# Optimization experiments

Hardware: AMD Instinct MI355X
Metric: run time of the kernel (lower is better)

Reference implementation:

```python
import jax, jax.numpy as jnp
import numpy as np

N_NODES = 100000
N_EDGES = 1600000
IN_C, HID_C, OUT_C = 64, 64, 40


def setup_inputs() -> dict:
    key = jax.random.key(0)
    ks = jax.random.split(key, 8)
    x = jax.random.normal(ks[0], (N_NODES, IN_C), dtype=jnp.float32)
    edge_index = jax.random.randint(ks[1], (2, N_EDGES), 0, N_NODES, dtype=jnp.int32)
    s = 1.0 / np.sqrt(HID_C)
    W1 = jax.random.uniform(ks[2], (IN_C, HID_C), jnp.float32, -s, s)
    b1 = jnp.zeros((HID_C,), jnp.float32)
    Wh = jax.random.uniform(ks[3], (HID_C, HID_C), jnp.float32, -s, s)
    bh = jnp.zeros((HID_C,), jnp.float32)
    W2 = jax.random.uniform(ks[4], (HID_C, OUT_C), jnp.float32, -s, s)
    b2 = jnp.zeros((OUT_C,), jnp.float32)
    return {"x": x, "edge_index": edge_index, "W1": W1, "b1": b1,
            "Wh": Wh, "bh": bh, "W2": W2, "b2": b2}


def reference(x, edge_index, W1, b1, Wh, bh, W2, b2):
    N = x.shape[0]
    loop = jnp.arange(N, dtype=edge_index.dtype)
    # GCN normalization with self-loops: A_hat = D^-1/2 (A + I) D^-1/2
    src = jnp.concatenate([edge_index[0], loop])  # [E + N]
    dst = jnp.concatenate([edge_index[1], loop])
    deg = jax.ops.segment_sum(jnp.ones_like(dst, dtype=x.dtype), dst, num_segments=N)
    dinv = jnp.where(deg > 0, jax.lax.rsqrt(deg), 0.0)
    norm = dinv[src] * dinv[dst]  # [E + N]

    def gcn_conv(h, W, b):
        h = h @ W                              # [N, out]
        msg = h[src] * norm[:, None]           # gather + scale, [E+N, out]
        return jax.ops.segment_sum(msg, dst, num_segments=N) + b

    h = jax.nn.relu(gcn_conv(x, W1, b1))       # conv1 (dropout = identity in eval)
    h = jax.nn.relu(gcn_conv(h, Wh, bh))       # hidden_conv, layer_size=2 -> one pass
    h = gcn_conv(h, W2, b2)                    # conv2
    return jax.nn.log_softmax(h, axis=1)
```

## Files before the change

kernel.cpp:

```cpp
#include <hip/hip_runtime.h>
#include <hip/hip_bf16.h>
#include <math.h>

#define EPT 16
#define BCAP 16384

typedef _Float16 half8 __attribute__((ext_vector_type(8)));
typedef _Float16 half2v __attribute__((ext_vector_type(2)));
typedef float f32x4 __attribute__((ext_vector_type(4)));

__device__ __forceinline__ unsigned short f16r(float f) {
    _Float16 h = (_Float16)f;
    return __builtin_bit_cast(unsigned short, h);
}
__device__ __forceinline__ half2v h2(unsigned u) {
    return __builtin_bit_cast(half2v, u);
}


__global__ void scat1_kernel(const int* __restrict__ src, const int* __restrict__ dst,
                             int* __restrict__ cntg, unsigned* __restrict__ ebuf, int E) {
    __shared__ int lh[256];
    __shared__ int lbase[256];
    int tid = threadIdx.x;
    lh[tid] = 0;
    __syncthreads();
    int base = blockIdx.x * (256 * EPT);
    int ds[EPT], ss[EPT];
#pragma unroll
    for (int k = 0; k < EPT; ++k) {
        int e = base + k * 256 + tid;
        ds[k] = (e < E) ? dst[e] : -1;
        ss[k] = (e < E) ? src[e] : 0;
    }
#pragma unroll
    for (int k = 0; k < EPT; ++k) {
        if (ds[k] >= 0) atomicAdd(&lh[ds[k] >> 9], 1);
    }
    __syncthreads();
    if (lh[tid] > 0) lbase[tid] = atomicAdd(&cntg[tid], lh[tid]);
    lh[tid] = 0;
    __syncthreads();
#pragma unroll
    for (int k = 0; k < EPT; ++k) {
        if (ds[k] >= 0) {
            int b = ds[k] >> 9;
            int pos = lbase[b] + atomicAdd(&lh[b], 1);
            ebuf[(size_t)b * BCAP + pos] = ((unsigned)ss[k] << 9) | (unsigned)(ds[k] & 511);
        }
    }
}

__global__ void build_kernel(const unsigned* __restrict__ ebuf, const int* __restrict__ cntg,
                             int* __restrict__ row_ptr, int* __restrict__ col,
                             float* __restrict__ dinv, int N, int E) {
    __shared__ int deg[512];
    __shared__ int sh[256];
    int b = blockIdx.x;
    int tid = threadIdx.x;

    int v = cntg[tid];
    sh[tid] = v;
    __syncthreads();
    int val = v;
    for (int off = 1; off < 256; off <<= 1) {
        int add = 0;
        if (tid >= off) add = sh[tid - off];
        __syncthreads();
        val += add;
        sh[tid] = val;
        __syncthreads();
    }
    int start = (b > 0) ? sh[b - 1] : 0;
    int cnt = cntg[b];
    __syncthreads();

    int nodeBase = b << 9;
    int nn = N - nodeBase;
    if (nn > 512) nn = 512;
    if (nn < 0) nn = 0;
    const unsigned* eb = ebuf + (size_t)b * BCAP;

    deg[tid] = 0;
    deg[tid + 256] = 0;
    __syncthreads();
    for (int j = tid; j < cnt; j += 256) {
        atomicAdd(&deg[eb[j] & 511u], 1);
    }
    __syncthreads();

    int i0 = tid * 2, i1 = i0 + 1;
    int v0 = deg[i0], v1 = deg[i1];
    int tot = v0 + v1;
    sh[tid] = tot;
    __syncthreads();
    int val2 = tot;
    for (int off = 1; off < 256; off <<= 1) {
        int add = 0;
        if (tid >= off) add = sh[tid - off];
        __syncthreads();
        val2 += add;
        sh[tid] = val2;
        __syncthreads();
    }
    int excl = val2 - tot;

    if (i0 < nn) { row_ptr[nodeBase + i0] = start + excl;      dinv[nodeBase + i0] = rsqrtf((float)v0 + 1.0f); }
    if (i1 < nn) { row_ptr[nodeBase + i1] = start + excl + v0; dinv[nodeBase + i1] = rsqrtf((float)v1 + 1.0f); }
    if (b == 0 && tid == 0) row_ptr[N] = E;
    deg[i0] = start + excl;
    deg[i1] = start + excl + v0;
    __syncthreads();

    for (int j = tid; j < cnt; j += 256) {
        unsigned rec = eb[j];
        int pos = atomicAdd(&deg[rec & 511u], 1);
        col[pos] = (int)(rec >> 9);
    }
}


__global__ void cvtpack_kernel(const float* __restrict__ x, unsigned short* __restrict__ xb,
                               int n4, int npad, const float* __restrict__ dinv,
                               const float* __restrict__ W1, const float* __restrict__ Wh,
                               const float* __restrict__ W2, unsigned short* __restrict__ wp1,
                               unsigned short* __restrict__ wph, unsigned short* __restrict__ wp2) {
    int bid = blockIdx.x;
    if (bid < 16) {
        int i = bid * 256 + threadIdx.x;
        int j = i & 7;
        int lane = (i >> 3) & 63;
        int hh = (i >> 9) & 1;
        int t = i >> 10;
        int k = hh * 32 + (lane >> 4) * 8 + j;
        int cc = t * 16 + (lane & 15);
        wp1[i] = f16r(W1[k * 64 + cc]);
        wph[i] = f16r(Wh[k * 64 + cc]);
        if (t < 3) wp2[i] = f16r(cc < 40 ? W2[k * 40 + cc] : 0.f);
    } else {
        if (bid == 16 && threadIdx.x < 8) {
            *(uint4*)(xb + (size_t)npad * 64 + threadIdx.x * 8) = make_uint4(0, 0, 0, 0);
        }
        int i = (bid - 16) * 256 + threadIdx.x;
        if (i < n4) {
            float dn = dinv[i >> 4];
            float4 v = *(const float4*)(x + (size_t)i * 4);
            ushort4 o;
            o.x = f16r(v.x * dn); o.y = f16r(v.y * dn);
            o.z = f16r(v.z * dn); o.w = f16r(v.w * dn);
            *(ushort4*)(xb + (size_t)i * 4) = o;
        }
    }
}


__launch_bounds__(256, 8)
__global__ void agg_kernel(const unsigned short* __restrict__ h, const int* __restrict__ row_ptr,
                           const int* __restrict__ col, const float* __restrict__ dinv,
                           unsigned short* __restrict__ aggout, int n, int zrow) {
    int tid = threadIdx.x;
    int lane = tid & 63;
    int node = blockIdx.x * 4 + (tid >> 6);
    if (node >= n) return;

    int sub = lane >> 3;
    unsigned choff = (lane & 7) * 16u;

    int beg = row_ptr[node];
    int deg = row_ptr[node + 1] - beg;
    float di = dinv[node];
    int total = deg + 1;

    half2v a0 = (half2v)0, a1 = (half2v)0, a2 = (half2v)0, a3 = (half2v)0;

    int base = 0;
    while (base < total) {
        int vi = base + lane;
        int idx = zrow;
        if (vi < deg) idx = col[beg + vi];
        else if (vi == deg) idx = node;
        int cnt = min(total - base, 64);
#pragma unroll
        for (int it = 0; it < 4; ++it) {
            int c0 = it * 16;
            if (c0 >= cnt) break;
            int s0 = __shfl(idx, c0 + sub);
            int s1 = __shfl(idx, c0 + 8 + sub);
            uint4 u0 = *(const uint4*)((const char*)h + (((unsigned)s0 << 7) + choff));
            uint4 u1 = *(const uint4*)((const char*)h + (((unsigned)s1 << 7) + choff));
            a0 += h2(u0.x);  a1 += h2(u0.y);  a2 += h2(u0.z);  a3 += h2(u0.w);
            a0 += h2(u1.x);  a1 += h2(u1.y);  a2 += h2(u1.z);  a3 += h2(u1.w);
        }
        base += cnt;
    }
#pragma unroll
    for (int off = 8; off <= 32; off <<= 1) {
        a0 += __builtin_bit_cast(half2v, __shfl_xor(__builtin_bit_cast(int, a0), off));
        a1 += __builtin_bit_cast(half2v, __shfl_xor(__builtin_bit_cast(int, a1), off));
        a2 += __builtin_bit_cast(half2v, __shfl_xor(__builtin_bit_cast(int, a2), off));
        a3 += __builtin_bit_cast(half2v, __shfl_xor(__builtin_bit_cast(int, a3), off));
    }

    if (sub == 0) {
        half2v dih = __builtin_bit_cast(half2v, __builtin_amdgcn_cvt_pkrtz(di, di));
        a0 *= dih; a1 *= dih; a2 *= dih; a3 *= dih;
        uint4 o;
        o.x = __builtin_bit_cast(unsigned, a0);
        o.y = __builtin_bit_cast(unsigned, a1);
        o.z = __builtin_bit_cast(unsigned, a2);
        o.w = __builtin_bit_cast(unsigned, a3);
        *(uint4*)((char*)aggout + (((unsigned)node << 7) + choff)) = o;
    }
}


__global__ void gemm_relu_kernel(const unsigned short* __restrict__ A,
                                 const unsigned short* __restrict__ wp,
                                 const float* __restrict__ bias,
                                 const float* __restrict__ dinv,
                                 unsigned short* __restrict__ out, int nTiles, int n, int zrow) {
    if (blockIdx.x == 0 && threadIdx.x < 8) {
        *(uint4*)(out + (size_t)zrow * 64 + threadIdx.x * 8) = make_uint4(0, 0, 0, 0);
    }
    int wv = blockIdx.x * 4 + (threadIdx.x >> 6);
    int lane = threadIdx.x & 63;
    if (wv >= nTiles) return;
    int q = lane >> 4, c = lane & 15;

    half8 bfrag[4][2];
#pragma unroll
    for (int t = 0; t < 4; ++t)
#pragma unroll
        for (int hh = 0; hh < 2; ++hh)
            bfrag[t][hh] = *(const half8*)(wp + t * 1024 + hh * 512 + lane * 8);
    float bs[4];
#pragma unroll
    for (int t = 0; t < 4; ++t) bs[t] = bias[t * 16 + c];

    int nodeBase = wv * 16;
    const unsigned short* arow = A + (size_t)(nodeBase + c) * 64 + q * 8;
    half8 a0 = *(const half8*)(arow);
    half8 a1 = *(const half8*)(arow + 32);

    f32x4 acc[4];
#pragma unroll
    for (int t = 0; t < 4; ++t) {
        f32x4 z = {0.f, 0.f, 0.f, 0.f};
        z = __builtin_amdgcn_mfma_f32_16x16x32_f16(a0, bfrag[t][0], z, 0, 0, 0);
        z = __builtin_amdgcn_mfma_f32_16x16x32_f16(a1, bfrag[t][1], z, 0, 0, 0);
        acc[t] = z;
    }

#pragma unroll
    for (int r = 0; r < 4; ++r) {
        int node = nodeBase + q * 4 + r;
        if (node < n) {
            float dn = dinv[node];
            unsigned short* orow = out + (size_t)node * 64;
#pragma unroll
            for (int t = 0; t < 4; ++t)
                orow[t * 16 + c] = f16r(fmaxf(acc[t][r] + bs[t], 0.f) * dn);
        }
    }
}

__global__ void gemm_lsm_kernel(const unsigned short* __restrict__ A,
                                const unsigned short* __restrict__ wp,
                                const float* __restrict__ bias,
                                float* __restrict__ out, int nTiles, int n) {
    int wv = blockIdx.x * 4 + (threadIdx.x >> 6);
    int lane = threadIdx.x & 63;
    if (wv >= nTiles) return;
    int q = lane >> 4, c = lane & 15;
    bool v2ok = (c < 8);

    half8 bfrag[3][2];
#pragma unroll
    for (int t = 0; t < 3; ++t)
#pragma unroll
        for (int hh = 0; hh < 2; ++hh)
            bfrag[t][hh] = *(const half8*)(wp + t * 1024 + hh * 512 + lane * 8);
    float bs[3];
    bs[0] = bias[c];
    bs[1] = bias[16 + c];
    bs[2] = v2ok ? bias[32 + c] : 0.f;

    int nodeBase = wv * 16;
    const unsigned short* arow = A + (size_t)(nodeBase + c) * 64 + q * 8;
    half8 a0 = *(const half8*)(arow);
    half8 a1 = *(const half8*)(arow + 32);

    f32x4 acc[3];
#pragma unroll
    for (int t = 0; t < 3; ++t) {
        f32x4 z = {0.f, 0.f, 0.f, 0.f};
        z = __builtin_amdgcn_mfma_f32_16x16x32_f16(a0, bfrag[t][0], z, 0, 0, 0);
        z = __builtin_amdgcn_mfma_f32_16x16x32_f16(a1, bfrag[t][1], z, 0, 0, 0);
        acc[t] = z;
    }

#pragma unroll
    for (int r = 0; r < 4; ++r) {
        int node = nodeBase + q * 4 + r;
        if (node < n) {
            float v0 = acc[0][r] + bs[0];
            float v1 = acc[1][r] + bs[1];
            float v2 = v2ok ? (acc[2][r] + bs[2]) : -INFINITY;
            float m = fmaxf(fmaxf(v0, v1), v2);
#pragma unroll
            for (int off = 1; off <= 8; off <<= 1) m = fmaxf(m, __shfl_xor(m, off));
            float s = expf(v0 - m) + expf(v1 - m) + (v2ok ? expf(v2 - m) : 0.f);
#pragma unroll
            for (int off = 1; off <= 8; off <<= 1) s += __shfl_xor(s, off);
            float ls = m + logf(s);
            float* orow = out + (size_t)node * 40;
            orow[c] = v0 - ls;
            orow[16 + c] = v1 - ls;
            if (v2ok) orow[32 + c] = v2 - ls;
        }
    }
}


extern "C" void kernel_launch(void* const* d_in, const int* in_sizes, int n_in,
                              void* d_out, int out_size, void* d_ws, size_t ws_size,
                              hipStream_t stream) {
    const float* x  = (const float*)d_in[0];
    const int* ei   = (const int*)d_in[1];
    const float* W1 = (const float*)d_in[2];
    const float* b1 = (const float*)d_in[3];
    const float* Wh = (const float*)d_in[4];
    const float* bh = (const float*)d_in[5];
    const float* W2 = (const float*)d_in[6];
    const float* b2 = (const float*)d_in[7];
    float* out = (float*)d_out;

    const int N = in_sizes[0] / 64;
    const int E = in_sizes[1] / 2;
    const int nbuk = (N + 511) >> 9;
    const int nTiles = (N + 15) / 16;
    const int Npad = nTiles * 16;

    const int* srcp = ei;
    const int* dstp = ei + E;

    size_t off = 0;
    auto alloc = [&](size_t bytes) {
        size_t o = off;
        off = (off + bytes + 255) & ~(size_t)255;
        return o;
    };
    char* ws = (char*)d_ws;
    int*      cntg    = (int*)(ws + alloc(256 * 4));
    int*      row_ptr = (int*)(ws + alloc((size_t)(N + 1) * 4));
    float*    dinv    = (float*)(ws + alloc((size_t)N * 4));
    int*      col     = (int*)(ws + alloc((size_t)E * 4));
    unsigned* ebuf    = (unsigned*)(ws + alloc((size_t)nbuk * BCAP * 4));
    unsigned short* wp1  = (unsigned short*)(ws + alloc(4096 * 2));
    unsigned short* wph  = (unsigned short*)(ws + alloc(4096 * 2));
    unsigned short* wp2  = (unsigned short*)(ws + alloc(3072 * 2));
    unsigned short* xb   = (unsigned short*)(ws + alloc((size_t)(Npad + 1) * 64 * 2));
    unsigned short* aggA = (unsigned short*)(ws + alloc((size_t)Npad * 64 * 2));
    unsigned short* gA   = (unsigned short*)(ws + alloc((size_t)(Npad + 1) * 64 * 2));
    (void)ws_size;

    hipMemsetAsync(cntg, 0, 256 * 4, stream);

    const int ebGrid = (E + 256 * EPT - 1) / (256 * EPT);
    scat1_kernel<<<ebGrid, 256, 0, stream>>>(srcp, dstp, cntg, ebuf, E);
    build_kernel<<<nbuk, 256, 0, stream>>>(ebuf, cntg, row_ptr, col, dinv, N, E);

    const int n4 = N * 16;
    cvtpack_kernel<<<16 + (n4 + 255) / 256, 256, 0, stream>>>(x, xb, n4, Npad, dinv,
                                                              W1, Wh, W2, wp1, wph, wp2);

    const int aggGrid = (N + 3) / 4;
    const int gemmGrid = (nTiles + 3) / 4;

    agg_kernel<<<aggGrid, 256, 0, stream>>>(xb, row_ptr, col, dinv, aggA, N, Npad);
    gemm_relu_kernel<<<gemmGrid, 256, 0, stream>>>(aggA, wp1, b1, dinv, gA, nTiles, N, Npad);
    agg_kernel<<<aggGrid, 256, 0, stream>>>(gA, row_ptr, col, dinv, aggA, N, Npad);
    gemm_relu_kernel<<<gemmGrid, 256, 0, stream>>>(aggA, wph, bh, dinv, gA, nTiles, N, Npad);
    agg_kernel<<<aggGrid, 256, 0, stream>>>(gA, row_ptr, col, dinv, aggA, N, Npad);
    gemm_lsm_kernel<<<gemmGrid, 256, 0, stream>>>(aggA, wp2, b2, out, nTiles, N);
}
```

Measured before the change: 269.8 us.

## Fuse neighbor aggregation with MFMA GEMM per 16-node tile via shared memory

Each block now aggregates 16 nodes (4 per wave, sequentially) into a shared-memory tile, then runs the MFMA projection with bias, ReLU or log-softmax directly from LDS. This removes the intermediate aggregated buffer round-trip through global memory and halves the number of kernel launches per layer. The trade-off is less memory-level parallelism per wave, since nodes are processed one after another, plus a block barrier. The final layer also leaves three of the four waves idle during the GEMM.

```diff
diff --git a/kernel.cpp b/kernel.cpp
--- a/kernel.cpp
+++ b/kernel.cpp
@@ -155,122 +155,169 @@
 
 
 __launch_bounds__(256, 8)
-__global__ void agg_kernel(const unsigned short* __restrict__ h, const int* __restrict__ row_ptr,
-                           const int* __restrict__ col, const float* __restrict__ dinv,
-                           unsigned short* __restrict__ aggout, int n, int zrow) {
+__global__ void fused_relu_kernel(const unsigned short* __restrict__ h,
+                                  const int* __restrict__ row_ptr,
+                                  const int* __restrict__ col,
+                                  const float* __restrict__ dinv,
+                                  const unsigned short* __restrict__ wp,
+                                  const float* __restrict__ bias,
+                                  unsigned short* __restrict__ out,
+                                  int n, int zrow) {
+    __shared__ unsigned short tile[16][72];
+    if (blockIdx.x == 0 && threadIdx.x < 8) {
+        *(uint4*)(out + (size_t)zrow * 64 + threadIdx.x * 8) = make_uint4(0, 0, 0, 0);
+    }
     int tid = threadIdx.x;
+    int w = tid >> 6;
     int lane = tid & 63;
-    int node = blockIdx.x * 4 + (tid >> 6);
-    if (node >= n) return;
-
     int sub = lane >> 3;
     unsigned choff = (lane & 7) * 16u;
-
-    int beg = row_ptr[node];
-    int deg = row_ptr[node + 1] - beg;
-    float di = dinv[node];
-    int total = deg + 1;
-
-    half2v a0 = (half2v)0, a1 = (half2v)0, a2 = (half2v)0, a3 = (half2v)0;
-
-    int base = 0;
-    while (base < total) {
-        int vi = base + lane;
-        int idx = zrow;
-        if (vi < deg) idx = col[beg + vi];
-        else if (vi == deg) idx = node;
-        int cnt = min(total - base, 64);
-#pragma unroll
-        for (int it = 0; it < 4; ++it) {
-            int c0 = it * 16;
-            if (c0 >= cnt) break;
-            int s0 = __shfl(idx, c0 + sub);
-            int s1 = __shfl(idx, c0 + 8 + sub);
-            uint4 u0 = *(const uint4*)((const char*)h + (((unsigned)s0 << 7) + choff));
-            uint4 u1 = *(const uint4*)((const char*)h + (((unsigned)s1 << 7) + choff));
-            a0 += h2(u0.x);  a1 += h2(u0.y);  a2 += h2(u0.z);  a3 += h2(u0.w);
-            a0 += h2(u1.x);  a1 += h2(u1.y);  a2 += h2(u1.z);  a3 += h2(u1.w);
-        }
-        base += cnt;
-    }
-#pragma unroll
-    for (int off = 8; off <= 32; off <<= 1) {
-        a0 += __builtin_bit_cast(half2v, __shfl_xor(__builtin_bit_cast(int, a0), off));
-        a1 += __builtin_bit_cast(half2v, __shfl_xor(__builtin_bit_cast(int, a1), off));
-        a2 += __builtin_bit_cast(half2v, __shfl_xor(__builtin_bit_cast(int, a2), off));
-        a3 += __builtin_bit_cast(half2v, __shfl_xor(__builtin_bit_cast(int, a3), off));
-    }
-
-    if (sub == 0) {
-        half2v dih = __builtin_bit_cast(half2v, __builtin_amdgcn_cvt_pkrtz(di, di));
-        a0 *= dih; a1 *= dih; a2 *= dih; a3 *= dih;
-        uint4 o;
-        o.x = __builtin_bit_cast(unsigned, a0);
-        o.y = __builtin_bit_cast(unsigned, a1);
-        o.z = __builtin_bit_cast(unsigned, a2);
-        o.w = __builtin_bit_cast(unsigned, a3);
-        *(uint4*)((char*)aggout + (((unsigned)node << 7) + choff)) = o;
-    }
-}
-
-
-__global__ void gemm_relu_kernel(const unsigned short* __restrict__ A,
-                                 const unsigned short* __restrict__ wp,
-                                 const float* __restrict__ bias,
-                                 const float* __restrict__ dinv,
-                                 unsigned short* __restrict__ out, int nTiles, int n, int zrow) {
-    if (blockIdx.x == 0 && threadIdx.x < 8) {
-        *(uint4*)(out + (size_t)zrow * 64 + threadIdx.x * 8) = make_uint4(0, 0, 0, 0);
-    }
-    int wv = blockIdx.x * 4 + (threadIdx.x >> 6);
-    int lane = threadIdx.x & 63;
-    if (wv >= nTiles) return;
+    int nodeBase = blockIdx.x * 16;
+
+#pragma unroll 1
+    for (int i = 0; i < 4; ++i) {
+        int row = w * 4 + i;
+        int node = nodeBase + row;
+        half2v a0 = (half2v)0, a1 = (half2v)0, a2 = (half2v)0, a3 = (half2v)0;
+        if (node < n) {
+            int beg = row_ptr[node];
+            int deg = row_ptr[node + 1] - beg;
+            float di = dinv[node];
+            int total = deg + 1;
+            int base = 0;
+            while (base < total) {
+                int vi = base + lane;
+                int idx = zrow;
+                if (vi < deg) idx = col[beg + vi];
+                else if (vi == deg) idx = node;
+                int cnt = min(total - base, 64);
+#pragma unroll
+                for (int it = 0; it < 4; ++it) {
+                    int c0 = it * 16;
+                    if (c0 >= cnt) break;
+                    int s0 = __shfl(idx, c0 + sub);
+                    int s1 = __shfl(idx, c0 + 8 + sub);
+                    uint4 u0 = *(const uint4*)((const char*)h + (((unsigned)s0 << 7) + choff));
+                    uint4 u1 = *(const uint4*)((const char*)h + (((unsigned)s1 << 7) + choff));
+                    a0 += h2(u0.x);  a1 += h2(u0.y);  a2 += h2(u0.z);  a3 += h2(u0.w);
+                    a0 += h2(u1.x);  a1 += h2(u1.y);  a2 += h2(u1.z);  a3 += h2(u1.w);
+                }
+                base += cnt;
+            }
+#pragma unroll
+            for (int off = 8; off <= 32; off <<= 1) {
+                a0 += __builtin_bit_cast(half2v, __shfl_xor(__builtin_bit_cast(int, a0), off));
+                a1 += __builtin_bit_cast(half2v, __shfl_xor(__builtin_bit_cast(int, a1), off));
+                a2 += __builtin_bit_cast(half2v, __shfl_xor(__builtin_bit_cast(int, a2), off));
+                a3 += __builtin_bit_cast(half2v, __shfl_xor(__builtin_bit_cast(int, a3), off));
+            }
+            if (sub == 0) {
+                half2v dih = __builtin_bit_cast(half2v, __builtin_amdgcn_cvt_pkrtz(di, di));
+                a0 *= dih; a1 *= dih; a2 *= dih; a3 *= dih;
+                uint4 o;
+                o.x = __builtin_bit_cast(unsigned, a0);
+                o.y = __builtin_bit_cast(unsigned, a1);
+                o.z = __builtin_bit_cast(unsigned, a2);
+                o.w = __builtin_bit_cast(unsigned, a3);
+                *(uint4*)((char*)&tile[row][0] + choff) = o;
+            }
+        } else if (sub == 0) {
+            *(uint4*)((char*)&tile[row][0] + choff) = make_uint4(0, 0, 0, 0);
+        }
+    }
+    __syncthreads();
+
     int q = lane >> 4, c = lane & 15;
-
-    half8 bfrag[4][2];
-#pragma unroll
-    for (int t = 0; t < 4; ++t)
-#pragma unroll
-        for (int hh = 0; hh < 2; ++hh)
-            bfrag[t][hh] = *(const half8*)(wp + t * 1024 + hh * 512 + lane * 8);
-    float bs[4];
-#pragma unroll
-    for (int t = 0; t < 4; ++t) bs[t] = bias[t * 16 + c];
-
-    int nodeBase = wv * 16;
-    const unsigned short* arow = A + (size_t)(nodeBase + c) * 64 + q * 8;
-    half8 a0 = *(const half8*)(arow);
-    half8 a1 = *(const half8*)(arow + 32);
-
-    f32x4 acc[4];
-#pragma unroll
-    for (int t = 0; t < 4; ++t) {
-        f32x4 z = {0.f, 0.f, 0.f, 0.f};
-        z = __builtin_amdgcn_mfma_f32_16x16x32_f16(a0, bfrag[t][0], z, 0, 0, 0);
-        z = __builtin_amdgcn_mfma_f32_16x16x32_f16(a1, bfrag[t][1], z, 0, 0, 0);
-        acc[t] = z;
-    }
-
+    half8 bf0 = *(const half8*)(wp + w * 1024 + lane * 8);
+    half8 bf1 = *(const half8*)(wp + w * 1024 + 512 + lane * 8);
+    float bs = bias[w * 16 + c];
+    half8 a0 = *(const half8*)&tile[c][q * 8];
+    half8 a1 = *(const half8*)&tile[c][32 + q * 8];
+    f32x4 z = {0.f, 0.f, 0.f, 0.f};
+    z = __builtin_amdgcn_mfma_f32_16x16x32_f16(a0, bf0, z, 0, 0, 0);
+    z = __builtin_amdgcn_mfma_f32_16x16x32_f16(a1, bf1, z, 0, 0, 0);
 #pragma unroll
     for (int r = 0; r < 4; ++r) {
         int node = nodeBase + q * 4 + r;
         if (node < n) {
             float dn = dinv[node];
-            unsigned short* orow = out + (size_t)node * 64;
-#pragma unroll
-            for (int t = 0; t < 4; ++t)
-                orow[t * 16 + c] = f16r(fmaxf(acc[t][r] + bs[t], 0.f) * dn);
-        }
-    }
-}
-
-__global__ void gemm_lsm_kernel(const unsigned short* __restrict__ A,
-                                const unsigned short* __restrict__ wp,
-                                const float* __restrict__ bias,
-                                float* __restrict__ out, int nTiles, int n) {
-    int wv = blockIdx.x * 4 + (threadIdx.x >> 6);
-    int lane = threadIdx.x & 63;
-    if (wv >= nTiles) return;
+            out[(size_t)node * 64 + w * 16 + c] = f16r(fmaxf(z[r] + bs, 0.f) * dn);
+        }
+    }
+}
+
+
+__launch_bounds__(256, 8)
+__global__ void fused_lsm_kernel(const unsigned short* __restrict__ h,
+                                 const int* __restrict__ row_ptr,
+                                 const int* __restrict__ col,
+                                 const float* __restrict__ dinv,
+                                 const unsigned short* __restrict__ wp,
+                                 const float* __restrict__ bias,
+                                 float* __restrict__ out,
+                                 int n, int zrow) {
+    __shared__ unsigned short tile[16][72];
+    int tid = threadIdx.x;
+    int w = tid >> 6;
+    int lane = tid & 63;
+    int sub = lane >> 3;
+    unsigned choff = (lane & 7) * 16u;
+    int nodeBase = blockIdx.x * 16;
+
+#pragma unroll 1
+    for (int i = 0; i < 4; ++i) {
+        int row = w * 4 + i;
+        int node = nodeBase + row;
+        half2v a0 = (half2v)0, a1 = (half2v)0, a2 = (half2v)0, a3 = (half2v)0;
+        if (node < n) {
+            int beg = row_ptr[node];
+            int deg = row_ptr[node + 1] - beg;
+            float di = dinv[node];
+            int total = deg + 1;
+            int base = 0;
+            while (base < total) {
+                int vi = base + lane;
+                int idx = zrow;
+                if (vi < deg) idx = col[beg + vi];
+                else if (vi == deg) idx = node;
+                int cnt = min(total - base, 64);
+#pragma unroll
+                for (int it = 0; it < 4; ++it) {
+                    int c0 = it * 16;
+                    if (c0 >= cnt) break;
+                    int s0 = __shfl(idx, c0 + sub);
+                    int s1 = __shfl(idx, c0 + 8 + sub);
+                    uint4 u0 = *(const uint4*)((const char*)h + (((unsigned)s0 << 7) + choff));
+                    uint4 u1 = *(const uint4*)((const char*)h + (((unsigned)s1 << 7) + choff));
+                    a0 += h2(u0.x);  a1 += h2(u0.y);  a2 += h2(u0.z);  a3 += h2(u0.w);
+                    a0 += h2(u1.x);  a1 += h2(u1.y);  a2 += h2(u1.z);  a3 += h2(u1.w);
+                }
+                base += cnt;
+            }
+#pragma unroll
+            for (int off = 8; off <= 32; off <<= 1) {
+                a0 += __builtin_bit_cast(half2v, __shfl_xor(__builtin_bit_cast(int, a0), off));
+                a1 += __builtin_bit_cast(half2v, __shfl_xor(__builtin_bit_cast(int, a1), off));
+                a2 += __builtin_bit_cast(half2v, __shfl_xor(__builtin_bit_cast(int, a2), off));
+                a3 += __builtin_bit_cast(half2v, __shfl_xor(__builtin_bit_cast(int, a3), off));
+            }
+            if (sub == 0) {
+                half2v dih = __builtin_bit_cast(half2v, __builtin_amdgcn_cvt_pkrtz(di, di));
+                a0 *= dih; a1 *= dih; a2 *= dih; a3 *= dih;
+                uint4 o;
+                o.x = __builtin_bit_cast(unsigned, a0);
+                o.y = __builtin_bit_cast(unsigned, a1);
+                o.z = __builtin_bit_cast(unsigned, a2);
+                o.w = __builtin_bit_cast(unsigned, a3);
+                *(uint4*)((char*)&tile[row][0] + choff) = o;
+            }
+        } else if (sub == 0) {
+            *(uint4*)((char*)&tile[row][0] + choff) = make_uint4(0, 0, 0, 0);
+        }
+    }
+    __syncthreads();
+    if (w != 0) return;
+
     int q = lane >> 4, c = lane & 15;
     bool v2ok = (c < 8);
 
@@ -285,10 +332,8 @@
     bs[1] = bias[16 + c];
     bs[2] = v2ok ? bias[32 + c] : 0.f;
 
-    int nodeBase = wv * 16;
-    const unsigned short* arow = A + (size_t)(nodeBase + c) * 64 + q * 8;
-    half8 a0 = *(const half8*)(arow);
-    half8 a1 = *(const half8*)(arow + 32);
+    half8 a0 = *(const half8*)&tile[c][q * 8];
+    half8 a1 = *(const half8*)&tile[c][32 + q * 8];
 
     f32x4 acc[3];
 #pragma unroll
@@ -360,8 +405,8 @@
     unsigned short* wph  = (unsigned short*)(ws + alloc(4096 * 2));
     unsigned short* wp2  = (unsigned short*)(ws + alloc(3072 * 2));
     unsigned short* xb   = (unsigned short*)(ws + alloc((size_t)(Npad + 1) * 64 * 2));
-    unsigned short* aggA = (unsigned short*)(ws + alloc((size_t)Npad * 64 * 2));
     unsigned short* gA   = (unsigned short*)(ws + alloc((size_t)(Npad + 1) * 64 * 2));
+    unsigned short* gB   = (unsigned short*)(ws + alloc((size_t)(Npad + 1) * 64 * 2));
     (void)ws_size;
 
     hipMemsetAsync(cntg, 0, 256 * 4, stream);
@@ -374,13 +419,7 @@
     cvtpack_kernel<<<16 + (n4 + 255) / 256, 256, 0, stream>>>(x, xb, n4, Npad, dinv,
                                                               W1, Wh, W2, wp1, wph, wp2);
 
-    const int aggGrid = (N + 3) / 4;
-    const int gemmGrid = (nTiles + 3) / 4;
-
-    agg_kernel<<<aggGrid, 256, 0, stream>>>(xb, row_ptr, col, dinv, aggA, N, Npad);
-    gemm_relu_kernel<<<gemmGrid, 256, 0, stream>>>(aggA, wp1, b1, dinv, gA, nTiles, N, Npad);
-    agg_kernel<<<aggGrid, 256, 0, stream>>>(gA, row_ptr, col, dinv, aggA, N, Npad);
-    gemm_relu_kernel<<<gemmGrid, 256, 0, stream>>>(aggA, wph, bh, dinv, gA, nTiles, N, Npad);
-    agg_kernel<<<aggGrid, 256, 0, stream>>>(gA, row_ptr, col, dinv, aggA, N, Npad);
-    gemm_lsm_kernel<<<gemmGrid, 256, 0, stream>>>(aggA, wp2, b2, out, nTiles, N);
-}
+    fused_relu_kernel<<<nTiles, 256, 0, stream>>>(xb, row_ptr, col, dinv, wp1, b1, gA, N, Npad);
+    fused_relu_kernel<<<nTiles, 256, 0, stream>>>(gA, row_ptr, col, dinv, wph, bh, gB, N, Npad);
+    fused_lsm_kernel<<<nTiles, 256, 0, stream>>>(gB, row_ptr, col, dinv, wp2, b2, out, N, Npad);
+}
```

Measured after the change: 252.0 us. -6.6%, faster.
